# Kernel optimization log

Measured on AMD Instinct MI355X. Metric: run time of the kernel, lower is better.

Reference implementation:

```python
import jax, jax.numpy as jnp
import numpy as np

B, T, C = 64, 512, 1024
D = C // 2  # split_len1 == split_len2
CLAMP = 5.0


def e(s):
    # exp(clamp * 0.636 * atan(s / clamp))
    return jnp.exp(CLAMP * 0.636 * jnp.arctan(s / CLAMP))


def gru_cell(x, h, Wih, Whh, bih, bhh):
    # Standard GRU cell, gate order (r, z, n) as in torch.nn.GRUCell.
    gi = x @ Wih.T + bih  # [B, 3D]
    gh = h @ Whh.T + bhh  # [B, 3D]
    i_r, i_z, i_n = gi[:, :D], gi[:, D:2 * D], gi[:, 2 * D:]
    h_r, h_z, h_n = gh[:, :D], gh[:, D:2 * D], gh[:, 2 * D:]
    r = jax.nn.sigmoid(i_r + h_r)
    z = jax.nn.sigmoid(i_z + h_z)
    n = jnp.tanh(i_n + r * h_n)
    return (1.0 - z) * n + z * h


def setup_inputs() -> dict:
    key = jax.random.key(0)
    ks = jax.random.split(key, 20)

    def p(k, shape, scale=0.05):
        return jax.random.normal(k, shape, jnp.float32) * scale

    inp = {"x": jax.random.normal(ks[0], (B, T, C), jnp.float32)}
    for i, name in enumerate(["s1", "s2"]):
        b = 1 + i * 6
        inp[f"{name}_Wih"] = p(ks[b], (3 * D, D))
        inp[f"{name}_Whh"] = p(ks[b + 1], (3 * D, D))
        inp[f"{name}_bih"] = p(ks[b + 2], (3 * D,))
        inp[f"{name}_bhh"] = p(ks[b + 3], (3 * D,))
        inp[f"{name}_Wo"] = p(ks[b + 4], (2 * D, D))
        inp[f"{name}_bo"] = p(ks[b + 5], (2 * D,))
    inp["cg1_W"] = p(ks[13], (D, D))
    inp["cg1_b"] = p(ks[14], (D,))
    inp["cg2_W"] = p(ks[15], (D, D))
    inp["cg2_b"] = p(ks[16], (D,))
    return inp


def reference(x, s1_Wih, s1_Whh, s1_bih, s1_bhh, s1_Wo, s1_bo,
              s2_Wih, s2_Whh, s2_bih, s2_bhh, s2_Wo, s2_bo,
              cg1_W, cg1_b, cg2_W, cg2_b):
    batch = x.shape[0]

    def step(carry, xt):
        h1, h2 = carry
        x1, x2 = xt[:, :D], xt[:, D:]
        # s2 GRU block on x2
        h2n = gru_cell(x2, h2, s2_Wih, s2_Whh, s2_bih, s2_bhh)
        r2 = h2n @ s2_Wo.T + s2_bo
        s2v, t2 = r2[:, :D], r2[:, D:]
        y1 = e(s2v) * x1 + t2
        # gate x2 with cg1 of OLD h1
        x2g = x2 * e(h1 @ cg1_W.T + cg1_b)
        # s1 GRU block on y1
        h1n = gru_cell(y1, h1, s1_Wih, s1_Whh, s1_bih, s1_bhh)
        r1 = h1n @ s1_Wo.T + s1_bo
        s1v, t1 = r1[:, :D], r1[:, D:]
        y2 = e(s1v) * x2g + t1
        # gate y1 with cg2 of OLD h2
        y1o = y1 * e(h2 @ cg2_W.T + cg2_b)
        return (h1n, h2n), jnp.concatenate([y1o, y2], axis=1)

    h0 = (jnp.zeros((batch, D), x.dtype), jnp.zeros((batch, D), x.dtype))
    _, ys = jax.lax.scan(step, h0, jnp.swapaxes(x, 0, 1))  # [T, B, C]
    return jnp.swapaxes(ys, 0, 1)  # [B, T, C]
```

## Files before the change

kernel.cpp:

```cpp
#include <hip/hip_runtime.h>
#include <math.h>

constexpr int kT = 512;
constexpr int kC = 1024;
constexpr int kD = 512;

typedef __attribute__((ext_vector_type(8))) short bf16x8;
typedef __attribute__((ext_vector_type(4))) float f32x4;
typedef __attribute__((ext_vector_type(4))) unsigned int u32x4;

__device__ __forceinline__ float b2f(unsigned short u) {
  unsigned int v = ((unsigned int)u) << 16;
  return __builtin_bit_cast(float, v);
}
__device__ __forceinline__ unsigned short f2b(float f) {
  unsigned int u = __builtin_bit_cast(unsigned int, f);
  u += 0x7fffu + ((u >> 16) & 1u);
  return (unsigned short)(u >> 16);
}
__device__ __forceinline__ float sigm(float x) {
  x = fminf(15.f, fmaxf(-15.f, x));
  return 1.f / (1.f + __expf(-x));
}
__device__ __forceinline__ float tanh_(float x) {
  x = fminf(15.f, fmaxf(-15.f, x));
  float e2 = __expf(2.f * x);
  return (e2 - 1.f) / (e2 + 1.f);
}
__device__ __forceinline__ float efun(float s) {
  return __expf((5.0f * 0.636f) * atanf(s * 0.2f));
}

__device__ __forceinline__ void st_b16_wt(unsigned short* p, unsigned short v) {
  asm volatile("global_store_short %0, %1, off sc0 sc1" ::"v"(p),
               "v"((unsigned int)v)
               : "memory");
}

__device__ __forceinline__ void poll_ge(const unsigned int* p, unsigned int tgt) {
  while (__hip_atomic_load(p, __ATOMIC_RELAXED, __HIP_MEMORY_SCOPE_AGENT) < tgt)
    __builtin_amdgcn_s_sleep(1);
}
__device__ __forceinline__ void poll2_ge(const unsigned int* pa,
                                         const unsigned int* pb,
                                         unsigned int tgt) {
  for (;;) {
    unsigned int a =
        __hip_atomic_load(pa, __ATOMIC_RELAXED, __HIP_MEMORY_SCOPE_AGENT);
    unsigned int b =
        __hip_atomic_load(pb, __ATOMIC_RELAXED, __HIP_MEMORY_SCOPE_AGENT);
    if (a >= tgt && b >= tgt) return;
    __builtin_amdgcn_s_sleep(1);
  }
}

__global__ __launch_bounds__(256) void cvt_x2_kernel(
    const float* __restrict__ x, unsigned short* __restrict__ xb2) {
  const int idx = blockIdx.x * 256 + threadIdx.x;
  const int e = idx * 8;
  const int dd = e & 511;
  const int tb = e >> 9;
  const int b = tb & 63;
  const int t = tb >> 6;
  const float* src = x + ((size_t)b * kT + t) * kC + kD + dd;
  f32x4 v0 = *(const f32x4*)src;
  f32x4 v1 = *(const f32x4*)(src + 4);
  bf16x8 o;
#pragma unroll
  for (int j = 0; j < 4; j++) {
    o[j] = (short)f2b(v0[j]);
    o[j + 4] = (short)f2b(v1[j]);
  }
  *(bf16x8*)(xb2 + e) = o;
}

__global__ __launch_bounds__(256, 1) void fused_glow_kernel(
    const float* __restrict__ x, const unsigned short* __restrict__ xb2,
    const float* __restrict__ A_Wih, const float* __restrict__ A_Whh,
    const float* __restrict__ A_bih, const float* __restrict__ A_bhh,
    const float* __restrict__ A_Wo, const float* __restrict__ A_bo,
    const float* __restrict__ A_cgW, const float* __restrict__ A_cgb,
    const float* __restrict__ B_Wih, const float* __restrict__ B_Whh,
    const float* __restrict__ B_bih, const float* __restrict__ B_bhh,
    const float* __restrict__ B_Wo, const float* __restrict__ B_bo,
    const float* __restrict__ B_cgW, const float* __restrict__ B_cgb,
    unsigned short* __restrict__ y1buf, float* __restrict__ out,
    unsigned short* __restrict__ hbA, unsigned short* __restrict__ hbB,
    unsigned int* __restrict__ arrA, unsigned int* __restrict__ arrB) {
  const int g = blockIdx.x;
  const bool isA = (g < 64);
  const int gl = isA ? g : (g - 64);
  const int tid = threadIdx.x;
  const int w = tid >> 6;
  const int l = tid & 63;
  const int q = l & 15;
  const int kg = l >> 4;
  const bool lo = (q < 8);
  const int qm = q & 7;
  const int d = 8 * gl + qm;
  const int browbase = 16 * w + 4 * kg;
  const int arow = 16 * w + q;
  const int acol = kg * 8;

  const float* Wih = isA ? A_Wih : B_Wih;
  const float* Whh = isA ? A_Whh : B_Whh;
  const float* bih = isA ? A_bih : B_bih;
  const float* bhh = isA ? A_bhh : B_bhh;
  const float* Wo = isA ? A_Wo : B_Wo;
  const float* bo = isA ? A_bo : B_bo;
  const float* cgW = isA ? A_cgW : B_cgW;
  const float* cgb = isA ? A_cgb : B_cgb;
  unsigned short* hbuf = isA ? hbA : hbB;

  __shared__ __attribute__((aligned(16))) unsigned short wlds[80 * 512];
  for (int c = tid; c < 80 * 64; c += 256) {
    const int u = c >> 6, kb = c & 63;
    const int s8 = 8 * gl + (u & 7);
    const int sel = u >> 3;
    u32x4 v = {0u, 0u, 0u, 0u};
    if (sel < 9) {
      const float* wrp = (sel == 0)   ? Whh + (size_t)s8 * kD
                         : (sel == 1) ? Whh + (size_t)(512 + s8) * kD
                         : (sel == 2) ? Whh + (size_t)(1024 + s8) * kD
                         : (sel == 3) ? cgW + (size_t)s8 * kD
                         : (sel == 4) ? Wo + (size_t)s8 * kD
                         : (sel == 5) ? Wo + (size_t)(512 + s8) * kD
                         : (sel == 6) ? Wih + (size_t)s8 * kD
                         : (sel == 7) ? Wih + (size_t)(512 + s8) * kD
                                      : Wih + (size_t)(1024 + s8) * kD;
      const float* p = wrp + kb * 8;
#pragma unroll
      for (int j = 0; j < 4; j++)
        v[j] = (unsigned int)f2b(p[2 * j]) | ((unsigned int)f2b(p[2 * j + 1]) << 16);
    }
    const int byteoff = u * 1024 + ((kb * 16) ^ ((u & 7) << 4));
    *(u32x4*)((char*)wlds + byteoff) = v;
  }

  float biasv[5];
  biasv[0] = lo ? bhh[d] : bhh[512 + d];
  biasv[1] = lo ? bhh[1024 + d] : cgb[d];
  biasv[2] = lo ? bo[d] : bo[512 + d];
  biasv[3] = lo ? bih[d] : bih[512 + d];
  biasv[4] = lo ? bih[1024 + d] : 0.f;

  float hsl[4] = {0.f, 0.f, 0.f, 0.f};
  float ecp[4];
#pragma unroll
  for (int r = 0; r < 4; r++) ecp[r] = efun(cgb[d]);

  __syncthreads();

  const int sw = qm << 4;
  const int s0 = isA ? 0 : 2;
  const int s1 = isA ? 512 : 514;
#pragma unroll 1
  for (int s = s0; s <= s1; ++s) {
    const int it = isA ? s : (s - 2);

    bf16x8 ax[16];
    float xopf[4] = {0.f, 0.f, 0.f, 0.f};
    if (isA) {
      const int itc = it < 511 ? it : 511;
      const unsigned short* xp = xb2 + ((size_t)itc * 64 + arow) * 512 + acol;
#pragma unroll
      for (int kk = 0; kk < 16; kk++) ax[kk] = *(const bf16x8*)(xp + kk * 32);
      if (lo) {
        const int ttc = s >= 1 ? s - 1 : 0;
#pragma unroll
        for (int r = 0; r < 4; r++)
          xopf[r] = x[(size_t)(browbase + r) * (kT * kC) + (size_t)ttc * kC + d];
      }
      if (s >= 1) {
        if (tid == 0) poll_ge(arrA + (s - 1), 64u);
        __syncthreads();
      }
    } else {
      if (lo) {
        const int ttc = it >= 1 ? it - 1 : 0;
#pragma unroll
        for (int r = 0; r < 4; r++)
          xopf[r] =
              x[(size_t)(browbase + r) * (kT * kC) + (size_t)ttc * kC + kD + d];
      }
      if (tid == 0) {
        const unsigned int* pa = arrA + (s - 1 < 512 ? s - 1 : 512);
        if (s >= 3)
          poll2_ge(pa, arrB + (s - 1), 64u);
        else
          poll_ge(pa, 64u);
      }
      __syncthreads();
      const int ity = it < 511 ? it : 511;
      const unsigned short* yp = y1buf + ((size_t)ity * 64 + arow) * 512 + acol;
#pragma unroll
      for (int kk = 0; kk < 16; kk++) ax[kk] = *(const bf16x8*)(yp + kk * 32);
    }

    const unsigned short* hp =
        hbuf + (size_t)(isA ? s : it) * 32768 + (size_t)arow * 512 + acol;
    bf16x8 ah[16];
#pragma unroll
    for (int kk = 0; kk < 16; kk++) ah[kk] = *(const bf16x8*)(hp + kk * 32);

    f32x4 acc0 = {0.f, 0.f, 0.f, 0.f}, acc1 = {0.f, 0.f, 0.f, 0.f};
    f32x4 acc2 = {0.f, 0.f, 0.f, 0.f}, acc3 = {0.f, 0.f, 0.f, 0.f};
    f32x4 acc4 = {0.f, 0.f, 0.f, 0.f};
#pragma unroll
    for (int kk = 0; kk < 16; kk++) {
      const int kbyte = (kk * 32 + kg * 8) * 2;
      bf16x8 b0 = *(const bf16x8*)((const char*)wlds + q * 1024 + (kbyte ^ sw));
      bf16x8 b1 =
          *(const bf16x8*)((const char*)wlds + (16 + q) * 1024 + (kbyte ^ sw));
      bf16x8 b2 =
          *(const bf16x8*)((const char*)wlds + (32 + q) * 1024 + (kbyte ^ sw));
      bf16x8 b3 =
          *(const bf16x8*)((const char*)wlds + (48 + q) * 1024 + (kbyte ^ sw));
      bf16x8 b4 =
          *(const bf16x8*)((const char*)wlds + (64 + q) * 1024 + (kbyte ^ sw));
      acc0 = __builtin_amdgcn_mfma_f32_16x16x32_bf16(ah[kk], b0, acc0, 0, 0, 0);
      acc1 = __builtin_amdgcn_mfma_f32_16x16x32_bf16(ah[kk], b1, acc1, 0, 0, 0);
      acc2 = __builtin_amdgcn_mfma_f32_16x16x32_bf16(ah[kk], b2, acc2, 0, 0, 0);
      acc3 = __builtin_amdgcn_mfma_f32_16x16x32_bf16(ax[kk], b3, acc3, 0, 0, 0);
      acc4 = __builtin_amdgcn_mfma_f32_16x16x32_bf16(ax[kk], b4, acc4, 0, 0, 0);
    }
    float ab0[4], ab1[4], ab2[4], ab3[4], ab4[4];
#pragma unroll
    for (int r = 0; r < 4; r++) {
      ab0[r] = acc0[r] + biasv[0];
      ab1[r] = acc1[r] + biasv[1];
      ab2[r] = acc2[r] + biasv[2];
      ab3[r] = acc3[r] + biasv[3];
      ab4[r] = acc4[r] + biasv[4];
    }
    float ghz[4], tv[4], giz[4], ec_sh[4];
#pragma unroll
    for (int r = 0; r < 4; r++) {
      ghz[r] = __shfl_xor(ab0[r], 8, 64);
      tv[r] = __shfl_xor(ab2[r], 8, 64);
      giz[r] = __shfl_xor(ab3[r], 8, 64);
      ec_sh[r] = __shfl_xor(ecp[r], 8, 64);
    }
    const int tt = it - 1;
    if (lo) {
#pragma unroll
      for (int r = 0; r < 4; r++) {
        const int b = browbase + r;
        if (it >= 1) {
          const float es = efun(ab2[r]);
          const size_t ooff =
              (size_t)b * (kT * kC) + (size_t)tt * kC + (isA ? 0 : kD) + d;
          if (isA) {
            const float yv = es * xopf[r] + tv[r];
            out[ooff] = yv * ec_sh[r];
            st_b16_wt(y1buf + ((size_t)tt * 64 + b) * 512 + d, f2b(yv));
          } else {
            out[ooff] = es * (xopf[r] * ec_sh[r]) + tv[r];
          }
        }
        if (it <= 511) {
          const float rr = sigm(ab3[r] + ab0[r]);
          const float zz = sigm(giz[r] + ghz[r]);
          const float nn = tanh_(ab4[r] + rr * ab1[r]);
          const float hn = (1.f - zz) * nn + zz * hsl[r];
          hsl[r] = hn;
          st_b16_wt(hbuf + (size_t)(it + 1) * 32768 + (size_t)b * 512 + d,
                    f2b(hn));
        }
      }
    } else {
#pragma unroll
      for (int r = 0; r < 4; r++) ecp[r] = efun(ab1[r]);
    }

    asm volatile("s_waitcnt vmcnt(0)" ::: "memory");
    __syncthreads();
    if (tid == 0)
      __hip_atomic_fetch_add((isA ? arrA : arrB) + s, 1u, __ATOMIC_RELAXED,
                             __HIP_MEMORY_SCOPE_AGENT);
  }
}

extern "C" void kernel_launch(void* const* d_in, const int* in_sizes, int n_in,
                              void* d_out, int out_size, void* d_ws, size_t ws_size,
                              hipStream_t stream) {
  (void)in_sizes; (void)n_in; (void)out_size; (void)ws_size;
  const float* x = (const float*)d_in[0];
  const float* s1_Wih = (const float*)d_in[1];
  const float* s1_Whh = (const float*)d_in[2];
  const float* s1_bih = (const float*)d_in[3];
  const float* s1_bhh = (const float*)d_in[4];
  const float* s1_Wo = (const float*)d_in[5];
  const float* s1_bo = (const float*)d_in[6];
  const float* s2_Wih = (const float*)d_in[7];
  const float* s2_Whh = (const float*)d_in[8];
  const float* s2_bih = (const float*)d_in[9];
  const float* s2_bhh = (const float*)d_in[10];
  const float* s2_Wo = (const float*)d_in[11];
  const float* s2_bo = (const float*)d_in[12];
  const float* cg1_W = (const float*)d_in[13];
  const float* cg1_b = (const float*)d_in[14];
  const float* cg2_W = (const float*)d_in[15];
  const float* cg2_b = (const float*)d_in[16];
  float* out = (float*)d_out;
  char* ws = (char*)d_ws;

  unsigned short* xb2 = (unsigned short*)ws;
  unsigned short* y1b = (unsigned short*)(ws + 33554432);
  unsigned short* hbA = (unsigned short*)(ws + 67108864);
  unsigned short* hbB = (unsigned short*)(ws + 100728832);
  unsigned int* arrA = (unsigned int*)(ws + 134348800);
  unsigned int* arrB = arrA + 640;

  hipMemsetAsync(ws + 67108864, 0, 65536, stream);
  hipMemsetAsync(ws + 100728832, 0, 65536, stream);
  hipMemsetAsync(ws + 134348800, 0, 8192, stream);

  cvt_x2_kernel<<<8192, 256, 0, stream>>>(x, xb2);

  fused_glow_kernel<<<128, 256, 0, stream>>>(
      x, xb2,
      s2_Wih, s2_Whh, s2_bih, s2_bhh, s2_Wo, s2_bo, cg2_W, cg2_b,
      s1_Wih, s1_Whh, s1_bih, s1_bhh, s1_Wo, s1_bo, cg1_W, cg1_b,
      y1b, out, hbA, hbB, arrA, arrB);
}
```

Before: 4.067 ms.

## Replace atomic counter barriers with per-block step flags polled wave-wide

Swaps the per-step atomic fetch-add counters for one padded flag per block, each storing its completed step. A full wavefront polls all 64 flags in parallel with __all, instead of a single thread spinning on a contended counter. The B group now loads y1 before waiting on its own peers, so the two waits overlap a little. It also widens the LDS XOR swizzle from 8 to 16 rows to cut bank conflicts, and makes the output stores write-through. The aim is lower cross-block sync latency on every recurrent step, at the cost of more polling traffic and the risk of subtle ordering bugs.

Result: faster. 3.698 ms (-9.1%).

```diff
diff --git a/kernel.cpp b/kernel.cpp
--- a/kernel.cpp
+++ b/kernel.cpp
@@ -36,22 +36,13 @@
                "v"((unsigned int)v)
                : "memory");
 }
-
-__device__ __forceinline__ void poll_ge(const unsigned int* p, unsigned int tgt) {
-  while (__hip_atomic_load(p, __ATOMIC_RELAXED, __HIP_MEMORY_SCOPE_AGENT) < tgt)
-    __builtin_amdgcn_s_sleep(1);
-}
-__device__ __forceinline__ void poll2_ge(const unsigned int* pa,
-                                         const unsigned int* pb,
-                                         unsigned int tgt) {
-  for (;;) {
-    unsigned int a =
-        __hip_atomic_load(pa, __ATOMIC_RELAXED, __HIP_MEMORY_SCOPE_AGENT);
-    unsigned int b =
-        __hip_atomic_load(pb, __ATOMIC_RELAXED, __HIP_MEMORY_SCOPE_AGENT);
-    if (a >= tgt && b >= tgt) return;
-    __builtin_amdgcn_s_sleep(1);
-  }
+__device__ __forceinline__ void st_f32_wt(float* p, float v) {
+  asm volatile("global_store_dword %0, %1, off sc0 sc1" ::"v"(p), "v"(v)
+               : "memory");
+}
+
+__device__ __forceinline__ unsigned int ldflag(const unsigned int* p) {
+  return __hip_atomic_load(p, __ATOMIC_RELAXED, __HIP_MEMORY_SCOPE_AGENT);
 }
 
 __global__ __launch_bounds__(256) void cvt_x2_kernel(
@@ -86,7 +77,7 @@
     const float* __restrict__ B_cgW, const float* __restrict__ B_cgb,
     unsigned short* __restrict__ y1buf, float* __restrict__ out,
     unsigned short* __restrict__ hbA, unsigned short* __restrict__ hbB,
-    unsigned int* __restrict__ arrA, unsigned int* __restrict__ arrB) {
+    unsigned int* __restrict__ flagsA, unsigned int* __restrict__ flagsB) {
   const int g = blockIdx.x;
   const bool isA = (g < 64);
   const int gl = isA ? g : (g - 64);
@@ -111,6 +102,7 @@
   const float* cgW = isA ? A_cgW : B_cgW;
   const float* cgb = isA ? A_cgb : B_cgb;
   unsigned short* hbuf = isA ? hbA : hbB;
+  unsigned int* myflag = (isA ? flagsA : flagsB) + (size_t)gl * 32;
 
   __shared__ __attribute__((aligned(16))) unsigned short wlds[80 * 512];
   for (int c = tid; c < 80 * 64; c += 256) {
@@ -133,7 +125,7 @@
       for (int j = 0; j < 4; j++)
         v[j] = (unsigned int)f2b(p[2 * j]) | ((unsigned int)f2b(p[2 * j + 1]) << 16);
     }
-    const int byteoff = u * 1024 + ((kb * 16) ^ ((u & 7) << 4));
+    const int byteoff = u * 1024 + ((kb * 16) ^ ((u & 15) << 4));
     *(u32x4*)((char*)wlds + byteoff) = v;
   }
 
@@ -151,7 +143,7 @@
 
   __syncthreads();
 
-  const int sw = qm << 4;
+  const int sw = q << 4;
   const int s0 = isA ? 0 : 2;
   const int s1 = isA ? 512 : 514;
 #pragma unroll 1
@@ -172,7 +164,14 @@
           xopf[r] = x[(size_t)(browbase + r) * (kT * kC) + (size_t)ttc * kC + d];
       }
       if (s >= 1) {
-        if (tid == 0) poll_ge(arrA + (s - 1), 64u);
+        if (w == 0) {
+          const unsigned int* fp = flagsA + (size_t)l * 32;
+          unsigned int v = ldflag(fp);
+          while (!__all((int)(v >= (unsigned)s))) {
+            __builtin_amdgcn_s_sleep(1);
+            v = ldflag(fp);
+          }
+        }
         __syncthreads();
       }
     } else {
@@ -183,18 +182,31 @@
           xopf[r] =
               x[(size_t)(browbase + r) * (kT * kC) + (size_t)ttc * kC + kD + d];
       }
-      if (tid == 0) {
-        const unsigned int* pa = arrA + (s - 1 < 512 ? s - 1 : 512);
-        if (s >= 3)
-          poll2_ge(pa, arrB + (s - 1), 64u);
-        else
-          poll_ge(pa, 64u);
+      const unsigned int tgtA = (unsigned)(s <= 513 ? s : 513);
+      if (w == 0) {
+        const unsigned int* fp = flagsA + (size_t)l * 32;
+        unsigned int v = ldflag(fp);
+        while (!__all((int)(v >= tgtA))) {
+          __builtin_amdgcn_s_sleep(1);
+          v = ldflag(fp);
+        }
       }
       __syncthreads();
       const int ity = it < 511 ? it : 511;
       const unsigned short* yp = y1buf + ((size_t)ity * 64 + arow) * 512 + acol;
 #pragma unroll
       for (int kk = 0; kk < 16; kk++) ax[kk] = *(const bf16x8*)(yp + kk * 32);
+      if (s >= 3) {
+        if (w == 0) {
+          const unsigned int* fp = flagsB + (size_t)l * 32;
+          unsigned int v = ldflag(fp);
+          while (!__all((int)(v >= (unsigned)s))) {
+            __builtin_amdgcn_s_sleep(1);
+            v = ldflag(fp);
+          }
+        }
+        __syncthreads();
+      }
     }
 
     const unsigned short* hp =
@@ -248,14 +260,14 @@
         const int b = browbase + r;
         if (it >= 1) {
           const float es = efun(ab2[r]);
-          const size_t ooff =
-              (size_t)b * (kT * kC) + (size_t)tt * kC + (isA ? 0 : kD) + d;
+          float* op = out + (size_t)b * (kT * kC) + (size_t)tt * kC +
+                      (isA ? 0 : kD) + d;
           if (isA) {
             const float yv = es * xopf[r] + tv[r];
-            out[ooff] = yv * ec_sh[r];
+            st_f32_wt(op, yv * ec_sh[r]);
             st_b16_wt(y1buf + ((size_t)tt * 64 + b) * 512 + d, f2b(yv));
           } else {
-            out[ooff] = es * (xopf[r] * ec_sh[r]) + tv[r];
+            st_f32_wt(op, es * (xopf[r] * ec_sh[r]) + tv[r]);
           }
         }
         if (it <= 511) {
@@ -276,8 +288,8 @@
     asm volatile("s_waitcnt vmcnt(0)" ::: "memory");
     __syncthreads();
     if (tid == 0)
-      __hip_atomic_fetch_add((isA ? arrA : arrB) + s, 1u, __ATOMIC_RELAXED,
-                             __HIP_MEMORY_SCOPE_AGENT);
+      __hip_atomic_store(myflag, (unsigned)(s + 1), __ATOMIC_RELAXED,
+                         __HIP_MEMORY_SCOPE_AGENT);
   }
 }
 
@@ -309,12 +321,12 @@
   unsigned short* y1b = (unsigned short*)(ws + 33554432);
   unsigned short* hbA = (unsigned short*)(ws + 67108864);
   unsigned short* hbB = (unsigned short*)(ws + 100728832);
-  unsigned int* arrA = (unsigned int*)(ws + 134348800);
-  unsigned int* arrB = arrA + 640;
+  unsigned int* flagsA = (unsigned int*)(ws + 134348800);
+  unsigned int* flagsB = (unsigned int*)(ws + 134348800 + 8192);
 
   hipMemsetAsync(ws + 67108864, 0, 65536, stream);
   hipMemsetAsync(ws + 100728832, 0, 65536, stream);
-  hipMemsetAsync(ws + 134348800, 0, 8192, stream);
+  hipMemsetAsync(ws + 134348800, 0, 16384, stream);
 
   cvt_x2_kernel<<<8192, 256, 0, stream>>>(x, xb2);
 
@@ -322,5 +334,5 @@
       x, xb2,
       s2_Wih, s2_Whh, s2_bih, s2_bhh, s2_Wo, s2_bo, cg2_W, cg2_b,
       s1_Wih, s1_Whh, s1_bih, s1_bhh, s1_Wo, s1_bo, cg1_W, cg1_b,
-      y1b, out, hbA, hbB, arrA, arrB);
-}
+      y1b, out, hbA, hbB, flagsA, flagsB);
+}
```
